# Performance work log

Measured on AMD Instinct MI355X. Metric: run time of the kernel, lower is better.

The kernel has to match this reference:

```python
import jax, jax.numpy as jnp
import numpy as np

N_NODES = 100000
N_EDGES = 3200000
D_IN = 128
D_HID = 128
D_FF = 256
N_CLASSES = 26
N_GRAPHS = 512


def setup_inputs() -> dict:
    key = jax.random.key(0)
    ks = jax.random.split(key, 12)
    s = 0.05
    return {
        "x": jax.random.normal(ks[0], (N_NODES, D_IN), dtype=jnp.float32),
        "edge_index": jax.random.randint(ks[1], (2, N_EDGES), 0, N_NODES, dtype=jnp.int64),
        "batch": jnp.sort(jax.random.randint(ks[2], (N_NODES,), 0, N_GRAPHS, dtype=jnp.int64)),
        "W1": jax.random.normal(ks[3], (D_IN, D_HID), dtype=jnp.float32) * s,
        "b1": jnp.zeros((D_HID,), dtype=jnp.float32),
        "W2": jax.random.normal(ks[4], (D_HID, D_HID), dtype=jnp.float32) * s,
        "b2": jnp.zeros((D_HID,), dtype=jnp.float32),
        "W3": jax.random.normal(ks[5], (D_HID, D_HID), dtype=jnp.float32) * s,
        "b3": jnp.zeros((D_HID,), dtype=jnp.float32),
        "Wfc": jax.random.normal(ks[6], (D_HID, D_FF), dtype=jnp.float32) * s,
        "bfc": jnp.zeros((D_FF,), dtype=jnp.float32),
        "Wfc2": jax.random.normal(ks[7], (D_FF, N_CLASSES), dtype=jnp.float32) * s,
        "bfc2": jnp.zeros((N_CLASSES,), dtype=jnp.float32),
    }


def _gcn_layer(x, src, dst, norm, W, b):
    # GCNConv: h = x @ W; out[dst] += norm_e * h[src]; out += b
    h = x @ W                                   # [N, D]
    msg = h[src] * norm[:, None]                # [E+N, D] gather + scale
    agg = jax.ops.segment_sum(msg, dst, num_segments=N_NODES)
    return agg + b


def reference(x, edge_index, batch, W1, b1, W2, b2, W3, b3, Wfc, bfc, Wfc2, bfc2):
    # add self-loops (PyG GCNConv default) and compute symmetric normalization once
    loop = jnp.arange(N_NODES, dtype=edge_index.dtype)
    src = jnp.concatenate([edge_index[0], loop])
    dst = jnp.concatenate([edge_index[1], loop])
    deg = jax.ops.segment_sum(jnp.ones_like(dst, dtype=x.dtype), dst, num_segments=N_NODES)
    dinv = jnp.where(deg > 0, jax.lax.rsqrt(deg), 0.0)
    norm = dinv[src] * dinv[dst]               # D^{-1/2} A_hat D^{-1/2}

    h = jax.nn.relu(_gcn_layer(x, src, dst, norm, W1, b1))
    h = jax.nn.relu(_gcn_layer(h, src, dst, norm, W2, b2))
    h = jax.nn.relu(_gcn_layer(h, src, dst, norm, W3, b3))

    # global mean pool over graphs
    sums = jax.ops.segment_sum(h, batch, num_segments=N_GRAPHS)       # [G, D]
    cnts = jax.ops.segment_sum(jnp.ones((h.shape[0],), h.dtype), batch, num_segments=N_GRAPHS)
    pooled = sums / jnp.maximum(cnts, 1.0)[:, None]

    out = jax.nn.relu(pooled @ Wfc + bfc)       # dropout is identity at inference
    return out @ Wfc2 + bfc2                    # [G, num_classes]
```

## Files before the change

kernel.cpp:

```cpp
#include <hip/hip_runtime.h>
#include <hip/hip_bf16.h>

typedef __bf16 bf16;
typedef __attribute__((ext_vector_type(8))) __bf16 bf16x8;
typedef __attribute__((ext_vector_type(4))) float f32x4;

constexpr int N_NODES   = 100000;
constexpr int N_PAD     = 100032;
constexpr int D         = 128;
constexpr int D_FF      = 256;
constexpr int N_CLASSES = 26;
constexpr int N_GRAPHS  = 512;
constexpr int NB1       = 256;
constexpr int NBUCK     = (N_NODES + 511) / 512;

__device__ inline float2 bf2f(unsigned u) {
    float lo = __uint_as_float(u << 16);
    float hi = __uint_as_float(u & 0xffff0000u);
    return make_float2(lo, hi);
}


__global__ __launch_bounds__(1024) void p1_hist(const int* __restrict__ edst,
                                                int* __restrict__ gcount, int e) {
    __shared__ int cnt[NBUCK];
    for (int t = threadIdx.x; t < NBUCK; t += 1024) cnt[t] = 0;
    __syncthreads();
    int chunk = (e + NB1 - 1) / NB1;
    int lo = blockIdx.x * chunk;
    int hi = min(e, lo + chunk);
    for (int i = lo + threadIdx.x; i < hi; i += 1024)
        atomicAdd(&cnt[edst[i] >> 9], 1);
    __syncthreads();
    for (int t = threadIdx.x; t < NBUCK; t += 1024)
        gcount[t * NB1 + blockIdx.x] = cnt[t];
}

__global__ __launch_bounds__(256) void scan1(const int* __restrict__ in,
                                             int* out, int* bsum, int n) {
    __shared__ int sd[256];
    int i = blockIdx.x * 256 + threadIdx.x;
    int v = (i < n) ? in[i] : 0;
    sd[threadIdx.x] = v; __syncthreads();
    for (int off = 1; off < 256; off <<= 1) {
        int t = (threadIdx.x >= off) ? sd[threadIdx.x - off] : 0;
        __syncthreads();
        sd[threadIdx.x] += t;
        __syncthreads();
    }
    if (i < n) out[i + 1] = sd[threadIdx.x];
    if (threadIdx.x == 255) bsum[blockIdx.x] = sd[255];
}

__global__ __launch_bounds__(1024) void scan2(const int* __restrict__ bsum,
                                              int* boff, int nb) {
    __shared__ int sd[1024];
    int t = threadIdx.x;
    int v = (t < nb) ? bsum[t] : 0;
    sd[t] = v; __syncthreads();
    for (int off = 1; off < 1024; off <<= 1) {
        int x = (t >= off) ? sd[t - off] : 0;
        __syncthreads();
        sd[t] += x;
        __syncthreads();
    }
    if (t < nb) boff[t] = sd[t] - v;
}

__global__ void scan3(int* out, const int* __restrict__ boff, int n) {
    int i = blockIdx.x * 256 + threadIdx.x;
    if (i < n) out[i + 1] += boff[blockIdx.x];
    if (i == 0) out[0] = 0;
}

__global__ __launch_bounds__(1024) void p3_scatter(const int* __restrict__ esrc,
                                                   const int* __restrict__ edst,
                                                   const int* __restrict__ gbase,
                                                   int* __restrict__ ebuf, int e) {
    __shared__ int cur[NBUCK];
    for (int t = threadIdx.x; t < NBUCK; t += 1024)
        cur[t] = gbase[t * NB1 + blockIdx.x];
    __syncthreads();
    int chunk = (e + NB1 - 1) / NB1;
    int lo = blockIdx.x * chunk;
    int hi = min(e, lo + chunk);
    for (int i = lo + threadIdx.x; i < hi; i += 1024) {
        int d = edst[i], s = esrc[i];
        int pos = atomicAdd(&cur[d >> 9], 1);
        ebuf[pos] = (s << 9) | (d & 511);
    }
}

__global__ __launch_bounds__(1024) void p45_fill(const int* __restrict__ ebuf,
                                                 const int* __restrict__ gbase,
                                                 float* __restrict__ dinv,
                                                 int* __restrict__ rowptr,
                                                 int* __restrict__ csrc, int e, int n) {
    __shared__ int cnt[512];
    __shared__ int ps[512];
    __shared__ int cur[512];
    int b = blockIdx.x, t = threadIdx.x;
    if (t < 512) cnt[t] = 0;
    __syncthreads();
    int lo = gbase[b * NB1];
    int hi = (b + 1 < NBUCK) ? gbase[(b + 1) * NB1] : e;
    for (int i = lo + t; i < hi; i += 1024)
        atomicAdd(&cnt[ebuf[i] & 511], 1);
    __syncthreads();
    int a = (t < 512) ? cnt[t] : 0;
    if (t < 512) ps[t] = a;
    __syncthreads();
    for (int off = 1; off < 512; off <<= 1) {
        int v = (t >= off && t < 512) ? ps[t - off] : 0;
        __syncthreads();
        if (t < 512) ps[t] += v;
        __syncthreads();
    }
    if (t < 512) {
        int g0 = lo + ps[t] - a;
        int node = b * 512 + t;
        cur[t] = g0;
        if (node < n) {
            rowptr[node] = g0;
            dinv[node] = 1.0f / sqrtf((float)(a + 1));
        }
    }
    if (b == 0 && t == 0) rowptr[n] = e;
    __syncthreads();
    for (int i = lo + t; i < hi; i += 1024) {
        int pe = ebuf[i];
        int pos = atomicAdd(&cur[pe & 511], 1);
        csrc[pos] = pe >> 9;
    }
}

__global__ __launch_bounds__(576) void starts_kernel(const int* __restrict__ batch,
                                                     int* __restrict__ starts, int n) {
    int g = threadIdx.x;
    if (g > N_GRAPHS) return;
    int lo = 0, hi = n;
    while (lo < hi) {
        int mid = (lo + hi) >> 1;
        if (batch[mid] < g) lo = mid + 1; else hi = mid;
    }
    starts[g] = lo;
}


__global__ void castWT3_kernel(const float* __restrict__ W0,
                               const float* __restrict__ W1,
                               const float* __restrict__ W2,
                               bf16* __restrict__ WT3) {
    int n = blockIdx.x, l = blockIdx.y, k = threadIdx.x;
    const float* W = (l == 0) ? W0 : (l == 1) ? W1 : W2;
    WT3[l * D * D + n * D + k] = (bf16)W[k * D + n];
}

__global__ __launch_bounds__(256) void gemm_kernel(const bf16* __restrict__ A,
                                                   const bf16* __restrict__ WT,
                                                   bf16* __restrict__ C) {
    int wave = threadIdx.x >> 6;
    int lane = threadIdx.x & 63;
    int m16  = lane & 15;
    int quad = lane >> 4;
    int row0 = blockIdx.x * 64 + wave * 16;

    bf16x8 a[4];
    const bf16* arow = A + (row0 + m16) * D + quad * 8;
#pragma unroll
    for (int kt = 0; kt < 4; ++kt)
        a[kt] = *(const bf16x8*)(arow + kt * 32);

#pragma unroll
    for (int nt = 0; nt < 8; ++nt) {
        f32x4 acc = {0.f, 0.f, 0.f, 0.f};
        const bf16* brow = WT + (nt * 16 + m16) * D + quad * 8;
#pragma unroll
        for (int kt = 0; kt < 4; ++kt) {
            bf16x8 b = *(const bf16x8*)(brow + kt * 32);
            acc = __builtin_amdgcn_mfma_f32_16x16x32_bf16(a[kt], b, acc, 0, 0, 0);
        }
#pragma unroll
        for (int r = 0; r < 4; ++r)
            C[(row0 + quad * 4 + r) * D + nt * 16 + m16] = (bf16)acc[r];
    }
}

__global__ __launch_bounds__(256) void gemm_f32_kernel(const float* __restrict__ A,
                                                       const bf16* __restrict__ WT,
                                                       bf16* __restrict__ C, int n) {
    int wave = threadIdx.x >> 6;
    int lane = threadIdx.x & 63;
    int m16  = lane & 15;
    int quad = lane >> 4;
    int row0 = blockIdx.x * 64 + wave * 16;
    int arowi = row0 + m16;

    bf16x8 a[4];
    const float* arow = A + (size_t)arowi * D + quad * 8;
#pragma unroll
    for (int kt = 0; kt < 4; ++kt) {
        float4 f0 = make_float4(0.f, 0.f, 0.f, 0.f);
        float4 f1 = make_float4(0.f, 0.f, 0.f, 0.f);
        if (arowi < n) {
            f0 = *(const float4*)(arow + kt * 32);
            f1 = *(const float4*)(arow + kt * 32 + 4);
        }
        bf16x8 v = { (bf16)f0.x, (bf16)f0.y, (bf16)f0.z, (bf16)f0.w,
                     (bf16)f1.x, (bf16)f1.y, (bf16)f1.z, (bf16)f1.w };
        a[kt] = v;
    }

#pragma unroll
    for (int nt = 0; nt < 8; ++nt) {
        f32x4 acc = {0.f, 0.f, 0.f, 0.f};
        const bf16* brow = WT + (nt * 16 + m16) * D + quad * 8;
#pragma unroll
        for (int kt = 0; kt < 4; ++kt) {
            bf16x8 b = *(const bf16x8*)(brow + kt * 32);
            acc = __builtin_amdgcn_mfma_f32_16x16x32_bf16(a[kt], b, acc, 0, 0, 0);
        }
#pragma unroll
        for (int r = 0; r < 4; ++r)
            C[(row0 + quad * 4 + r) * D + nt * 16 + m16] = (bf16)acc[r];
    }
}

__global__ __launch_bounds__(256) void spmm_kernel(const bf16* __restrict__ h,
                                                   const int* __restrict__ rowptr,
                                                   const int* __restrict__ csrc,
                                                   const float* __restrict__ dinv,
                                                   const float* __restrict__ bias,
                                                   bf16* __restrict__ out, int n) {
    int v = blockIdx.x * 4 + (threadIdx.x >> 6);
    if (v >= n) return;
    int lane = threadIdx.x & 63;
    int g = lane >> 4;
    int c = lane & 15;
    int s = rowptr[v], e = rowptr[v + 1];
    float dv = dinv[v];

    float acc[8] = {0.f, 0.f, 0.f, 0.f, 0.f, 0.f, 0.f, 0.f};

    if (g == 0) {
        uint4 u = *(const uint4*)(h + v * D + c * 8);
        float s2 = dv * dv;
        float2 f0 = bf2f(u.x), f1 = bf2f(u.y), f2 = bf2f(u.z), f3 = bf2f(u.w);
        acc[0] = s2 * f0.x; acc[1] = s2 * f0.y;
        acc[2] = s2 * f1.x; acc[3] = s2 * f1.y;
        acc[4] = s2 * f2.x; acc[5] = s2 * f2.y;
        acc[6] = s2 * f3.x; acc[7] = s2 * f3.y;
    }

    int j = s + g;
    for (; j + 4 < e; j += 8) {
        int s0 = csrc[j], s1 = csrc[j + 4];
        float w0 = dinv[s0] * dv, w1 = dinv[s1] * dv;
        uint4 ua = *(const uint4*)(h + s0 * D + c * 8);
        uint4 ub = *(const uint4*)(h + s1 * D + c * 8);
        float2 a0 = bf2f(ua.x), a1 = bf2f(ua.y), a2 = bf2f(ua.z), a3 = bf2f(ua.w);
        float2 b0 = bf2f(ub.x), b1 = bf2f(ub.y), b2 = bf2f(ub.z), b3 = bf2f(ub.w);
        acc[0] = fmaf(w0, a0.x, acc[0]); acc[1] = fmaf(w0, a0.y, acc[1]);
        acc[2] = fmaf(w0, a1.x, acc[2]); acc[3] = fmaf(w0, a1.y, acc[3]);
        acc[4] = fmaf(w0, a2.x, acc[4]); acc[5] = fmaf(w0, a2.y, acc[5]);
        acc[6] = fmaf(w0, a3.x, acc[6]); acc[7] = fmaf(w0, a3.y, acc[7]);
        acc[0] = fmaf(w1, b0.x, acc[0]); acc[1] = fmaf(w1, b0.y, acc[1]);
        acc[2] = fmaf(w1, b1.x, acc[2]); acc[3] = fmaf(w1, b1.y, acc[3]);
        acc[4] = fmaf(w1, b2.x, acc[4]); acc[5] = fmaf(w1, b2.y, acc[5]);
        acc[6] = fmaf(w1, b3.x, acc[6]); acc[7] = fmaf(w1, b3.y, acc[7]);
    }
    if (j < e) {
        int s0 = csrc[j];
        float w0 = dinv[s0] * dv;
        uint4 ua = *(const uint4*)(h + s0 * D + c * 8);
        float2 a0 = bf2f(ua.x), a1 = bf2f(ua.y), a2 = bf2f(ua.z), a3 = bf2f(ua.w);
        acc[0] = fmaf(w0, a0.x, acc[0]); acc[1] = fmaf(w0, a0.y, acc[1]);
        acc[2] = fmaf(w0, a1.x, acc[2]); acc[3] = fmaf(w0, a1.y, acc[3]);
        acc[4] = fmaf(w0, a2.x, acc[4]); acc[5] = fmaf(w0, a2.y, acc[5]);
        acc[6] = fmaf(w0, a3.x, acc[6]); acc[7] = fmaf(w0, a3.y, acc[7]);
    }

#pragma unroll
    for (int d = 0; d < 8; ++d) {
        acc[d] += __shfl_xor(acc[d], 16);
        acc[d] += __shfl_xor(acc[d], 32);
    }

    if (g == 0) {
        float4 bi0 = *(const float4*)(bias + c * 8);
        float4 bi1 = *(const float4*)(bias + c * 8 + 4);
        bf16x8 o;
        o[0] = (bf16)fmaxf(acc[0] + bi0.x, 0.f);
        o[1] = (bf16)fmaxf(acc[1] + bi0.y, 0.f);
        o[2] = (bf16)fmaxf(acc[2] + bi0.z, 0.f);
        o[3] = (bf16)fmaxf(acc[3] + bi0.w, 0.f);
        o[4] = (bf16)fmaxf(acc[4] + bi1.x, 0.f);
        o[5] = (bf16)fmaxf(acc[5] + bi1.y, 0.f);
        o[6] = (bf16)fmaxf(acc[6] + bi1.z, 0.f);
        o[7] = (bf16)fmaxf(acc[7] + bi1.w, 0.f);
        *(bf16x8*)(out + v * D + c * 8) = o;
    }
}

__global__ __launch_bounds__(256) void poolfc_kernel(const bf16* __restrict__ h,
                                                     const int* __restrict__ starts,
                                                     const float* __restrict__ Wfc,
                                                     const float* __restrict__ bfc,
                                                     const float* __restrict__ Wfc2,
                                                     const float* __restrict__ bfc2,
                                                     float* __restrict__ out) {
    __shared__ float part[3][D];
    __shared__ float pr[D];
    __shared__ float hid[D_FF];
    int g = blockIdx.x;
    int w = threadIdx.x >> 6, lane = threadIdx.x & 63;
    int s = starts[g], e = starts[g + 1];
    float ax = 0.f, ay = 0.f;
    for (int r = s + w; r < e; r += 4) {
        unsigned u = *(const unsigned*)(h + r * D + lane * 2);
        float2 f = bf2f(u);
        ax += f.x; ay += f.y;
    }
    if (w > 0) { part[w - 1][lane * 2] = ax; part[w - 1][lane * 2 + 1] = ay; }
    __syncthreads();
    if (w == 0) {
#pragma unroll
        for (int k = 0; k < 3; ++k) { ax += part[k][lane * 2]; ay += part[k][lane * 2 + 1]; }
        float c = fmaxf((float)(e - s), 1.0f);
        pr[lane * 2]     = ax / c;
        pr[lane * 2 + 1] = ay / c;
    }
    __syncthreads();
    int t = threadIdx.x;
    float acc = bfc[t];
    for (int k = 0; k < D; ++k) acc = fmaf(pr[k], Wfc[k * D_FF + t], acc);
    hid[t] = fmaxf(acc, 0.f);
    __syncthreads();
    if (t < N_CLASSES) {
        float o = bfc2[t];
        for (int k = 0; k < D_FF; ++k) o = fmaf(hid[k], Wfc2[k * N_CLASSES + t], o);
        out[g * N_CLASSES + t] = o;
    }
}


extern "C" void kernel_launch(void* const* d_in, const int* in_sizes, int n_in,
                              void* d_out, int out_size, void* d_ws, size_t ws_size,
                              hipStream_t stream) {
    const float* x     = (const float*)d_in[0];
    const int*   eidx  = (const int*)d_in[1];
    const int*   batch = (const int*)d_in[2];
    const float* W[3]  = { (const float*)d_in[3], (const float*)d_in[5], (const float*)d_in[7] };
    const float* b[3]  = { (const float*)d_in[4], (const float*)d_in[6], (const float*)d_in[8] };
    const float* Wfc   = (const float*)d_in[9];
    const float* bfc   = (const float*)d_in[10];
    const float* Wfc2  = (const float*)d_in[11];
    const float* bfc2  = (const float*)d_in[12];
    float* out = (float*)d_out;

    const int E = in_sizes[1] / 2;
    const int N = in_sizes[0] / D;
    const int* esrc = eidx;
    const int* edst = eidx + E;

    uint8_t* base = (uint8_t*)d_ws;
    size_t off = 0;
    auto alloc = [&](size_t bytes) -> void* {
        void* p = base + off;
        off = (off + bytes + 255) & ~(size_t)255;
        return p;
    };
    bf16*  hA     = (bf16*) alloc((size_t)N_PAD * D * 2);
    bf16*  hB     = (bf16*) alloc((size_t)N_PAD * D * 2);
    bf16*  WT3    = (bf16*) alloc((size_t)3 * D * D * 2);
    int*   csrc   = (int*)  alloc((size_t)E * 4);
    int*   ebuf   = (int*)  alloc((size_t)E * 4);
    int*   gcount = (int*)  alloc((size_t)NBUCK * NB1 * 4);
    int*   gbase  = (int*)  alloc((size_t)(NBUCK * NB1 + 1) * 4);
    int*   rowptr = (int*)  alloc((size_t)(N + 1) * 4);
    float* dinv   = (float*)alloc((size_t)N * 4);
    int*   bsum   = (int*)  alloc(4096);
    int*   boff   = (int*)  alloc(4096);
    int*   starts = (int*)  alloc((size_t)(N_GRAPHS + 1) * 4);
    (void)ws_size; (void)n_in; (void)out_size;

    const int GB  = N_PAD / 64;
    const int SB  = (N + 3) / 4;
    const int GCN = NBUCK * NB1;
    const int GCB = (GCN + 255) / 256;

    p1_hist<<<NB1, 1024, 0, stream>>>(edst, gcount, E);
    scan1<<<GCB, 256, 0, stream>>>(gcount, gbase, bsum, GCN);
    scan2<<<1, 1024, 0, stream>>>(bsum, boff, GCB);
    scan3<<<GCB, 256, 0, stream>>>(gbase, boff, GCN);
    p3_scatter<<<NB1, 1024, 0, stream>>>(esrc, edst, gbase, ebuf, E);
    p45_fill<<<NBUCK, 1024, 0, stream>>>(ebuf, gbase, dinv, rowptr, csrc, E, N);

    starts_kernel<<<1, 576, 0, stream>>>(batch, starts, N);

    castWT3_kernel<<<dim3(D, 3), D, 0, stream>>>(W[0], W[1], W[2], WT3);

    gemm_f32_kernel<<<GB, 256, 0, stream>>>(x, WT3, hA, N);
    spmm_kernel<<<SB, 256, 0, stream>>>(hA, rowptr, csrc, dinv, b[0], hB, N);
    for (int l = 1; l < 3; ++l) {
        gemm_kernel<<<GB, 256, 0, stream>>>(hB, WT3 + (size_t)l * D * D, hA);
        spmm_kernel<<<SB, 256, 0, stream>>>(hA, rowptr, csrc, dinv, b[l], hB, N);
    }

    poolfc_kernel<<<N_GRAPHS, 256, 0, stream>>>(hB, starts, Wfc, bfc, Wfc2, bfc2, out);
}
```

Baseline: 632.8 us.

## Fold source-side dinv into GEMM epilogue and merge small setup kernels

The GEMM epilogues now pre-scale each output row by dinv[row], so the SpMM gather no longer loads dinv[src] per edge and only applies dv once at the end. The SpMM loop is unrolled to four gathers in flight. The scan2, scan3, starts and weight-cast kernels are merged into one misc kernel, with block offsets added where they are consumed, which cuts launches. The final FC layer in the pooling kernel is parallelised across threads. This trades a small change in rounding order (the scale is applied before the bf16 cast) for fewer random loads and fewer launches.

```diff
diff --git a/kernel.cpp b/kernel.cpp
--- a/kernel.cpp
+++ b/kernel.cpp
@@ -48,38 +48,57 @@
         sd[threadIdx.x] += t;
         __syncthreads();
     }
-    if (i < n) out[i + 1] = sd[threadIdx.x];
+    if (i < n) out[i] = sd[threadIdx.x] - v;
     if (threadIdx.x == 255) bsum[blockIdx.x] = sd[255];
 }
 
-__global__ __launch_bounds__(1024) void scan2(const int* __restrict__ bsum,
-                                              int* boff, int nb) {
-    __shared__ int sd[1024];
+__global__ __launch_bounds__(1024) void misc_kernel(const int* __restrict__ bsum,
+                                                    int* __restrict__ boff, int nb,
+                                                    const int* __restrict__ batch,
+                                                    int* __restrict__ starts, int n,
+                                                    const float* __restrict__ W0,
+                                                    const float* __restrict__ W1,
+                                                    const float* __restrict__ W2,
+                                                    bf16* __restrict__ WT3) {
     int t = threadIdx.x;
-    int v = (t < nb) ? bsum[t] : 0;
-    sd[t] = v; __syncthreads();
-    for (int off = 1; off < 1024; off <<= 1) {
-        int x = (t >= off) ? sd[t - off] : 0;
-        __syncthreads();
-        sd[t] += x;
-        __syncthreads();
-    }
-    if (t < nb) boff[t] = sd[t] - v;
-}
-
-__global__ void scan3(int* out, const int* __restrict__ boff, int n) {
-    int i = blockIdx.x * 256 + threadIdx.x;
-    if (i < n) out[i + 1] += boff[blockIdx.x];
-    if (i == 0) out[0] = 0;
+    if (blockIdx.x == 0) {
+        if (t <= N_GRAPHS) {
+            int lo = 0, hi = n;
+            while (lo < hi) {
+                int mid = (lo + hi) >> 1;
+                if (batch[mid] < t) lo = mid + 1; else hi = mid;
+            }
+            starts[t] = lo;
+        }
+        __shared__ int sd[1024];
+        int v = (t < nb) ? bsum[t] : 0;
+        sd[t] = v; __syncthreads();
+        for (int off = 1; off < 1024; off <<= 1) {
+            int x = (t >= off) ? sd[t - off] : 0;
+            __syncthreads();
+            sd[t] += x;
+            __syncthreads();
+        }
+        if (t < nb) boff[t] = sd[t] - v;
+    } else {
+        int idx = (blockIdx.x - 1) * 1024 + t;
+        int l = idx >> 14;
+        int rem = idx & 16383;
+        int nn = rem >> 7;
+        int kk = rem & 127;
+        const float* W = (l == 0) ? W0 : (l == 1) ? W1 : W2;
+        WT3[idx] = (bf16)W[kk * D + nn];
+    }
 }
 
 __global__ __launch_bounds__(1024) void p3_scatter(const int* __restrict__ esrc,
                                                    const int* __restrict__ edst,
                                                    const int* __restrict__ gbase,
+                                                   const int* __restrict__ boff,
                                                    int* __restrict__ ebuf, int e) {
     __shared__ int cur[NBUCK];
     for (int t = threadIdx.x; t < NBUCK; t += 1024)
-        cur[t] = gbase[t * NB1 + blockIdx.x];
+        cur[t] = gbase[t * NB1 + blockIdx.x] + boff[t];
     __syncthreads();
     int chunk = (e + NB1 - 1) / NB1;
     int lo = blockIdx.x * chunk;
@@ -93,6 +112,7 @@
 
 __global__ __launch_bounds__(1024) void p45_fill(const int* __restrict__ ebuf,
                                                  const int* __restrict__ gbase,
+                                                 const int* __restrict__ boff,
                                                  float* __restrict__ dinv,
                                                  int* __restrict__ rowptr,
                                                  int* __restrict__ csrc, int e, int n) {
@@ -102,8 +122,8 @@
     int b = blockIdx.x, t = threadIdx.x;
     if (t < 512) cnt[t] = 0;
     __syncthreads();
-    int lo = gbase[b * NB1];
-    int hi = (b + 1 < NBUCK) ? gbase[(b + 1) * NB1] : e;
+    int lo = gbase[b * NB1] + boff[b];
+    int hi = (b + 1 < NBUCK) ? gbase[(b + 1) * NB1] + boff[b + 1] : e;
     for (int i = lo + t; i < hi; i += 1024)
         atomicAdd(&cnt[ebuf[i] & 511], 1);
     __syncthreads();
@@ -134,31 +154,11 @@
     }
 }
 
-__global__ __launch_bounds__(576) void starts_kernel(const int* __restrict__ batch,
-                                                     int* __restrict__ starts, int n) {
-    int g = threadIdx.x;
-    if (g > N_GRAPHS) return;
-    int lo = 0, hi = n;
-    while (lo < hi) {
-        int mid = (lo + hi) >> 1;
-        if (batch[mid] < g) lo = mid + 1; else hi = mid;
-    }
-    starts[g] = lo;
-}
-
-
-__global__ void castWT3_kernel(const float* __restrict__ W0,
-                               const float* __restrict__ W1,
-                               const float* __restrict__ W2,
-                               bf16* __restrict__ WT3) {
-    int n = blockIdx.x, l = blockIdx.y, k = threadIdx.x;
-    const float* W = (l == 0) ? W0 : (l == 1) ? W1 : W2;
-    WT3[l * D * D + n * D + k] = (bf16)W[k * D + n];
-}
 
 __global__ __launch_bounds__(256) void gemm_kernel(const bf16* __restrict__ A,
                                                    const bf16* __restrict__ WT,
-                                                   bf16* __restrict__ C) {
+                                                   bf16* __restrict__ C,
+                                                   const float* __restrict__ dinv, int n) {
     int wave = threadIdx.x >> 6;
     int lane = threadIdx.x & 63;
     int m16  = lane & 15;
@@ -171,6 +171,13 @@
     for (int kt = 0; kt < 4; ++kt)
         a[kt] = *(const bf16x8*)(arow + kt * 32);
 
+    float sc[4];
+#pragma unroll
+    for (int r = 0; r < 4; ++r) {
+        int rr = row0 + quad * 4 + r;
+        sc[r] = (rr < n) ? dinv[rr] : 0.f;
+    }
+
 #pragma unroll
     for (int nt = 0; nt < 8; ++nt) {
         f32x4 acc = {0.f, 0.f, 0.f, 0.f};
@@ -182,13 +189,14 @@
         }
 #pragma unroll
         for (int r = 0; r < 4; ++r)
-            C[(row0 + quad * 4 + r) * D + nt * 16 + m16] = (bf16)acc[r];
+            C[(row0 + quad * 4 + r) * D + nt * 16 + m16] = (bf16)(sc[r] * acc[r]);
     }
 }
 
 __global__ __launch_bounds__(256) void gemm_f32_kernel(const float* __restrict__ A,
                                                        const bf16* __restrict__ WT,
-                                                       bf16* __restrict__ C, int n) {
+                                                       bf16* __restrict__ C,
+                                                       const float* __restrict__ dinv, int n) {
     int wave = threadIdx.x >> 6;
     int lane = threadIdx.x & 63;
     int m16  = lane & 15;
@@ -211,6 +219,13 @@
         a[kt] = v;
     }
 
+    float sc[4];
+#pragma unroll
+    for (int r = 0; r < 4; ++r) {
+        int rr = row0 + quad * 4 + r;
+        sc[r] = (rr < n) ? dinv[rr] : 0.f;
+    }
+
 #pragma unroll
     for (int nt = 0; nt < 8; ++nt) {
         f32x4 acc = {0.f, 0.f, 0.f, 0.f};
@@ -222,7 +237,7 @@
         }
 #pragma unroll
         for (int r = 0; r < 4; ++r)
-            C[(row0 + quad * 4 + r) * D + nt * 16 + m16] = (bf16)acc[r];
+            C[(row0 + quad * 4 + r) * D + nt * 16 + m16] = (bf16)(sc[r] * acc[r]);
     }
 }
 
@@ -243,41 +258,46 @@
     float acc[8] = {0.f, 0.f, 0.f, 0.f, 0.f, 0.f, 0.f, 0.f};
 
     if (g == 0) {
-        uint4 u = *(const uint4*)(h + v * D + c * 8);
-        float s2 = dv * dv;
+        uint4 u = *(const uint4*)(h + (size_t)v * D + c * 8);
         float2 f0 = bf2f(u.x), f1 = bf2f(u.y), f2 = bf2f(u.z), f3 = bf2f(u.w);
-        acc[0] = s2 * f0.x; acc[1] = s2 * f0.y;
-        acc[2] = s2 * f1.x; acc[3] = s2 * f1.y;
-        acc[4] = s2 * f2.x; acc[5] = s2 * f2.y;
-        acc[6] = s2 * f3.x; acc[7] = s2 * f3.y;
+        acc[0] = f0.x; acc[1] = f0.y; acc[2] = f1.x; acc[3] = f1.y;
+        acc[4] = f2.x; acc[5] = f2.y; acc[6] = f3.x; acc[7] = f3.y;
     }
 
     int j = s + g;
-    for (; j + 4 < e; j += 8) {
-        int s0 = csrc[j], s1 = csrc[j + 4];
-        float w0 = dinv[s0] * dv, w1 = dinv[s1] * dv;
-        uint4 ua = *(const uint4*)(h + s0 * D + c * 8);
-        uint4 ub = *(const uint4*)(h + s1 * D + c * 8);
-        float2 a0 = bf2f(ua.x), a1 = bf2f(ua.y), a2 = bf2f(ua.z), a3 = bf2f(ua.w);
-        float2 b0 = bf2f(ub.x), b1 = bf2f(ub.y), b2 = bf2f(ub.z), b3 = bf2f(ub.w);
-        acc[0] = fmaf(w0, a0.x, acc[0]); acc[1] = fmaf(w0, a0.y, acc[1]);
-        acc[2] = fmaf(w0, a1.x, acc[2]); acc[3] = fmaf(w0, a1.y, acc[3]);
-        acc[4] = fmaf(w0, a2.x, acc[4]); acc[5] = fmaf(w0, a2.y, acc[5]);
-        acc[6] = fmaf(w0, a3.x, acc[6]); acc[7] = fmaf(w0, a3.y, acc[7]);
-        acc[0] = fmaf(w1, b0.x, acc[0]); acc[1] = fmaf(w1, b0.y, acc[1]);
-        acc[2] = fmaf(w1, b1.x, acc[2]); acc[3] = fmaf(w1, b1.y, acc[3]);
-        acc[4] = fmaf(w1, b2.x, acc[4]); acc[5] = fmaf(w1, b2.y, acc[5]);
-        acc[6] = fmaf(w1, b3.x, acc[6]); acc[7] = fmaf(w1, b3.y, acc[7]);
-    }
-    if (j < e) {
+    for (; j + 12 < e; j += 16) {
+        int s0 = csrc[j], s1 = csrc[j + 4], s2 = csrc[j + 8], s3 = csrc[j + 12];
+        uint4 u0 = *(const uint4*)(h + (size_t)s0 * D + c * 8);
+        uint4 u1 = *(const uint4*)(h + (size_t)s1 * D + c * 8);
+        uint4 u2 = *(const uint4*)(h + (size_t)s2 * D + c * 8);
+        uint4 u3 = *(const uint4*)(h + (size_t)s3 * D + c * 8);
+        {
+            float2 a0 = bf2f(u0.x), a1 = bf2f(u0.y), a2 = bf2f(u0.z), a3 = bf2f(u0.w);
+            acc[0] += a0.x; acc[1] += a0.y; acc[2] += a1.x; acc[3] += a1.y;
+            acc[4] += a2.x; acc[5] += a2.y; acc[6] += a3.x; acc[7] += a3.y;
+        }
+        {
+            float2 a0 = bf2f(u1.x), a1 = bf2f(u1.y), a2 = bf2f(u1.z), a3 = bf2f(u1.w);
+            acc[0] += a0.x; acc[1] += a0.y; acc[2] += a1.x; acc[3] += a1.y;
+            acc[4] += a2.x; acc[5] += a2.y; acc[6] += a3.x; acc[7] += a3.y;
+        }
+        {
+            float2 a0 = bf2f(u2.x), a1 = bf2f(u2.y), a2 = bf2f(u2.z), a3 = bf2f(u2.w);
+            acc[0] += a0.x; acc[1] += a0.y; acc[2] += a1.x; acc[3] += a1.y;
+            acc[4] += a2.x; acc[5] += a2.y; acc[6] += a3.x; acc[7] += a3.y;
+        }
+        {
+            float2 a0 = bf2f(u3.x), a1 = bf2f(u3.y), a2 = bf2f(u3.z), a3 = bf2f(u3.w);
+            acc[0] += a0.x; acc[1] += a0.y; acc[2] += a1.x; acc[3] += a1.y;
+            acc[4] += a2.x; acc[5] += a2.y; acc[6] += a3.x; acc[7] += a3.y;
+        }
+    }
+    for (; j < e; j += 4) {
         int s0 = csrc[j];
-        float w0 = dinv[s0] * dv;
-        uint4 ua = *(const uint4*)(h + s0 * D + c * 8);
-        float2 a0 = bf2f(ua.x), a1 = bf2f(ua.y), a2 = bf2f(ua.z), a3 = bf2f(ua.w);
-        acc[0] = fmaf(w0, a0.x, acc[0]); acc[1] = fmaf(w0, a0.y, acc[1]);
-        acc[2] = fmaf(w0, a1.x, acc[2]); acc[3] = fmaf(w0, a1.y, acc[3]);
-        acc[4] = fmaf(w0, a2.x, acc[4]); acc[5] = fmaf(w0, a2.y, acc[5]);
-        acc[6] = fmaf(w0, a3.x, acc[6]); acc[7] = fmaf(w0, a3.y, acc[7]);
+        uint4 u0 = *(const uint4*)(h + (size_t)s0 * D + c * 8);
+        float2 a0 = bf2f(u0.x), a1 = bf2f(u0.y), a2 = bf2f(u0.z), a3 = bf2f(u0.w);
+        acc[0] += a0.x; acc[1] += a0.y; acc[2] += a1.x; acc[3] += a1.y;
+        acc[4] += a2.x; acc[5] += a2.y; acc[6] += a3.x; acc[7] += a3.y;
     }
 
 #pragma unroll
@@ -290,14 +310,14 @@
         float4 bi0 = *(const float4*)(bias + c * 8);
         float4 bi1 = *(const float4*)(bias + c * 8 + 4);
         bf16x8 o;
-        o[0] = (bf16)fmaxf(acc[0] + bi0.x, 0.f);
-        o[1] = (bf16)fmaxf(acc[1] + bi0.y, 0.f);
-        o[2] = (bf16)fmaxf(acc[2] + bi0.z, 0.f);
-        o[3] = (bf16)fmaxf(acc[3] + bi0.w, 0.f);
-        o[4] = (bf16)fmaxf(acc[4] + bi1.x, 0.f);
-        o[5] = (bf16)fmaxf(acc[5] + bi1.y, 0.f);
-        o[6] = (bf16)fmaxf(acc[6] + bi1.z, 0.f);
-        o[7] = (bf16)fmaxf(acc[7] + bi1.w, 0.f);
+        o[0] = (bf16)fmaxf(fmaf(dv, acc[0], bi0.x), 0.f);
+        o[1] = (bf16)fmaxf(fmaf(dv, acc[1], bi0.y), 0.f);
+        o[2] = (bf16)fmaxf(fmaf(dv, acc[2], bi0.z), 0.f);
+        o[3] = (bf16)fmaxf(fmaf(dv, acc[3], bi0.w), 0.f);
+        o[4] = (bf16)fmaxf(fmaf(dv, acc[4], bi1.x), 0.f);
+        o[5] = (bf16)fmaxf(fmaf(dv, acc[5], bi1.y), 0.f);
+        o[6] = (bf16)fmaxf(fmaf(dv, acc[6], bi1.z), 0.f);
+        o[7] = (bf16)fmaxf(fmaf(dv, acc[7], bi1.w), 0.f);
         *(bf16x8*)(out + v * D + c * 8) = o;
     }
 }
@@ -312,6 +332,7 @@
     __shared__ float part[3][D];
     __shared__ float pr[D];
     __shared__ float hid[D_FF];
+    __shared__ float red[N_CLASSES][9];
     int g = blockIdx.x;
     int w = threadIdx.x >> 6, lane = threadIdx.x & 63;
     int s = starts[g], e = starts[g + 1];
@@ -332,13 +353,27 @@
     }
     __syncthreads();
     int t = threadIdx.x;
-    float acc = bfc[t];
-    for (int k = 0; k < D; ++k) acc = fmaf(pr[k], Wfc[k * D_FF + t], acc);
-    hid[t] = fmaxf(acc, 0.f);
+    float a0 = 0.f, a1 = 0.f, a2 = 0.f, a3 = 0.f;
+    for (int k = 0; k < D; k += 4) {
+        a0 = fmaf(pr[k],     Wfc[k * D_FF + t],       a0);
+        a1 = fmaf(pr[k + 1], Wfc[(k + 1) * D_FF + t], a1);
+        a2 = fmaf(pr[k + 2], Wfc[(k + 2) * D_FF + t], a2);
+        a3 = fmaf(pr[k + 3], Wfc[(k + 3) * D_FF + t], a3);
+    }
+    hid[t] = fmaxf((a0 + a1) + (a2 + a3) + bfc[t], 0.f);
+    __syncthreads();
+    if (t < N_CLASSES * 8) {
+        int cls = t >> 3, kk = t & 7;
+        float o = 0.f;
+        for (int k = kk; k < D_FF; k += 8)
+            o = fmaf(hid[k], Wfc2[k * N_CLASSES + cls], o);
+        red[cls][kk] = o;
+    }
     __syncthreads();
     if (t < N_CLASSES) {
         float o = bfc2[t];
-        for (int k = 0; k < D_FF; ++k) o = fmaf(hid[k], Wfc2[k * N_CLASSES + t], o);
+#pragma unroll
+        for (int k = 0; k < 8; ++k) o += red[t][k];
         out[g * N_CLASSES + t] = o;
     }
 }
@@ -391,19 +426,15 @@
 
     p1_hist<<<NB1, 1024, 0, stream>>>(edst, gcount, E);
     scan1<<<GCB, 256, 0, stream>>>(gcount, gbase, bsum, GCN);
-    scan2<<<1, 1024, 0, stream>>>(bsum, boff, GCB);
-    scan3<<<GCB, 256, 0, stream>>>(gbase, boff, GCN);
-    p3_scatter<<<NB1, 1024, 0, stream>>>(esrc, edst, gbase, ebuf, E);
-    p45_fill<<<NBUCK, 1024, 0, stream>>>(ebuf, gbase, dinv, rowptr, csrc, E, N);
-
-    starts_kernel<<<1, 576, 0, stream>>>(batch, starts, N);
-
-    castWT3_kernel<<<dim3(D, 3), D, 0, stream>>>(W[0], W[1], W[2], WT3);
-
-    gemm_f32_kernel<<<GB, 256, 0, stream>>>(x, WT3, hA, N);
+    misc_kernel<<<49, 1024, 0, stream>>>(bsum, boff, GCB, batch, starts, N,
+                                         W[0], W[1], W[2], WT3);
+    p3_scatter<<<NB1, 1024, 0, stream>>>(esrc, edst, gbase, boff, ebuf, E);
+    p45_fill<<<NBUCK, 1024, 0, stream>>>(ebuf, gbase, boff, dinv, rowptr, csrc, E, N);
+
+    gemm_f32_kernel<<<GB, 256, 0, stream>>>(x, WT3, hA, dinv, N);
     spmm_kernel<<<SB, 256, 0, stream>>>(hA, rowptr, csrc, dinv, b[0], hB, N);
     for (int l = 1; l < 3; ++l) {
-        gemm_kernel<<<GB, 256, 0, stream>>>(hB, WT3 + (size_t)l * D * D, hA);
+        gemm_kernel<<<GB, 256, 0, stream>>>(hB, WT3 + (size_t)l * D * D, hA, dinv, N);
         spmm_kernel<<<SB, 256, 0, stream>>>(hA, rowptr, csrc, dinv, b[l], hB, N);
     }
 
```

After: 632.4 us. About the same (-0.1%).
